# Optimization experiments

Hardware: AMD Instinct MI355X
Metric: run time of the kernel (lower is better)

## Reference

```python
import jax, jax.numpy as jnp
import numpy as np

LRELU = 0.01  # torch nn.LeakyReLU default slope

def _lrelu(x):
    return jnp.where(x >= 0, x, LRELU * x)

def setup_inputs() -> dict:
    key = jax.random.key(0)
    ks = jax.random.split(key, 10)
    B, Cin, Cout, H, W, K, FD, LAT = 16, 256, 256, 64, 64, 3, 128, 128
    y = jax.random.normal(ks[0], (B, Cin, H, W), jnp.float32)
    finger = jax.random.randint(ks[1], (B, FD), 0, 2).astype(jnp.float32)
    ori_weight = jax.random.normal(ks[2], (Cout, Cin, K, K), jnp.float32) * 0.05
    w_mask = jax.random.normal(ks[3], (Cout, Cin, 1, 1), jnp.float32)
    f_weight = ori_weight[None]  # param initialized as 1*ori_weight, shape [1,Cout,Cin,K,K]
    style_w1 = jax.random.normal(ks[4], (LAT, FD), jnp.float32) / np.sqrt(FD)
    style_w2 = jax.random.normal(ks[5], (2 * Cin * K * K, LAT), jnp.float32) / np.sqrt(LAT)
    ori_bias = jax.random.normal(ks[6], (Cout,), jnp.float32) * 0.05
    b_mask = jax.random.normal(ks[7], (Cout,), jnp.float32)
    f_bias = ori_bias[None]  # [1,Cout]
    bias_w1 = jax.random.normal(ks[8], (Cout, FD), jnp.float32) / np.sqrt(FD)
    bias_w2 = jax.random.normal(ks[9], (Cout, Cout), jnp.float32) / np.sqrt(Cout)
    return dict(y=y, finger=finger, ori_weight=ori_weight, w_mask=w_mask,
                f_weight=f_weight, style_w1=style_w1, style_w2=style_w2,
                ori_bias=ori_bias, b_mask=b_mask, f_bias=f_bias,
                bias_w1=bias_w1, bias_w2=bias_w2)

def reference(y, finger, ori_weight, w_mask, f_weight, style_w1, style_w2,
              ori_bias, b_mask, f_bias, bias_w1, bias_w2):
    B = y.shape[0]
    Cout, Cin, K, _ = ori_weight.shape
    relu6 = lambda v: jnp.clip(v, 0.0, 6.0)
    # mask blending coefficients (w_mask broadcasts over the KxK taps, as in .repeat)
    f_w_weight = (6.0 - relu6(w_mask)) / 6.0          # [Cout,Cin,1,1]
    f_w_bias = (6.0 - relu6(b_mask)) / 6.0            # [Cout]
    mean_ori = ori_weight.mean()
    std_ori = jnp.std(ori_weight, ddof=1)             # torch .std() is unbiased
    # ApplyStyle: finger -> LAT -> 2*Cin*K*K scale/shift applied to f_weight
    h = _lrelu(finger @ style_w1.T)                   # [B,LAT]
    style = (h @ style_w2.T).reshape(B, 2, 1, Cin, K, K)
    s_weight = f_weight * (style[:, 0] + 1.0) + style[:, 1]  # [B,Cout,Cin,K,K]
    fw = f_w_weight[None]
    w1 = (1.0 - fw) * ori_weight[None] + fw * s_weight
    # per-sample whole-tensor re-standardization to ori stats
    mean = w1.mean(axis=(1, 2, 3, 4), keepdims=True)
    std = jnp.std(w1, axis=(1, 2, 3, 4), keepdims=True, ddof=1)
    w2 = (w1 - mean) / std * std_ori + mean_ori
    new_weight = (1.0 - fw) * ori_weight[None] + fw * w2      # [B,Cout,Cin,K,K]
    # per-sample bias
    s_bias = f_bias * _lrelu(_lrelu(finger @ bias_w1.T) @ bias_w2.T)  # [B,Cout]
    new_bias = (1.0 - f_w_bias) * ori_bias + f_w_bias * s_bias        # [B,Cout]
    pad = K // 2
    def conv_one(xi, wi, bi):
        o = jax.lax.conv_general_dilated(xi[None], wi, (1, 1),
                                         [(pad, pad), (pad, pad)],
                                         dimension_numbers=('NCHW', 'OIHW', 'NCHW'))
        return o[0] + bi[:, None, None]
    return jax.vmap(conv_one)(y, new_weight, new_bias)   # [B,Cout,H,W]
```

## Files before the change

kernel.cpp:

```cpp
#include <hip/hip_runtime.h>
#include <math.h>

#define LSLOPE 0.01f

__device__ __forceinline__ float lrelu(float x){ return x >= 0.f ? x : LSLOPE * x; }

typedef __attribute__((ext_vector_type(8))) short short8;
typedef __attribute__((ext_vector_type(4))) float f32x4;

__device__ __forceinline__ unsigned short f2bf(float f){
  union { float f; unsigned u; } v; v.f = f;
  unsigned r = v.u + 0x7FFFu + ((v.u >> 16) & 1u);
  return (unsigned short)(r >> 16);
}

__device__ __forceinline__ void gload_lds16(const unsigned short* g, unsigned short* l){
  __builtin_amdgcn_global_load_lds((const __attribute__((address_space(1))) unsigned int*)(g),
                                   (__attribute__((address_space(3))) unsigned int*)(l), 16, 0, 0);
}

constexpr int B    = 16;
constexpr int CIN  = 256;
constexpr int COUT = 256;
constexpr int HH   = 64;
constexpr int WW   = 64;
constexpr int FD   = 128;
constexpr int LAT  = 128;
constexpr int WPS  = CIN * 9;
constexpr int WTOT = COUT * WPS;
constexpr int HP   = 66;

constexpr int OFF_STAT  = 0;
constexpr int OFF_BMEAN = 16;
constexpr int OFF_BSTD  = 32;
constexpr int OFF_P     = 64;
constexpr int OFF_C     = OFF_P + 11 * 8 * WPS;
constexpr int OFF_STYLE = OFF_C + 11 * WPS;
constexpr int OFF_NBIAS = OFF_STYLE + B * 2 * WPS;
constexpr int OFF_NW    = OFF_NBIAS + B * COUT;
constexpr int OFF_YTR   = OFF_NW + (B * 9 * COUT * CIN) / 2;

__global__ __launch_bounds__(256) void k_coeff(const float* __restrict__ ow, const float* __restrict__ fwgt,
                                               const float* __restrict__ wmask, float* __restrict__ P){
  const int rb = blockIdx.x, ob = blockIdx.y;
  const int tid = threadIdx.x;
  const int rem = rb * 256 + tid;
  const int ic = rem / 9;
  float a_ow = 0.f, q_ow = 0.f, ab = 0.f, qb = 0.f;
  float a1 = 0.f, a2 = 0.f, d1 = 0.f, d2 = 0.f, d3 = 0.f, d4 = 0.f, d5 = 0.f;
  for (int oc = ob * 32; oc < ob * 32 + 32; ++oc){
    float w = ow[(size_t)oc * WPS + rem];
    float f = fwgt[(size_t)oc * WPS + rem];
    float m = wmask[oc * CIN + ic];
    float fw = (6.f - fminf(fmaxf(m, 0.f), 6.f)) * (1.f / 6.f);
    float base = w + fw * (f - w);
    float c1 = fw * f, c2 = fw;
    a_ow += w; q_ow += w * w;
    ab += base; qb += base * base;
    a1 += c1; a2 += c2;
    d1 += c1 * c1; d2 += c2 * c2; d3 += base * c1; d4 += base * c2; d5 += c1 * c2;
  }
  float* p = P + (size_t)ob * WPS + rem;
  p[(size_t)0  * 8 * WPS] = a_ow; p[(size_t)1  * 8 * WPS] = q_ow;
  p[(size_t)2  * 8 * WPS] = ab;   p[(size_t)3  * 8 * WPS] = qb;
  p[(size_t)4  * 8 * WPS] = a1;   p[(size_t)5  * 8 * WPS] = a2;
  p[(size_t)6  * 8 * WPS] = d1;   p[(size_t)7  * 8 * WPS] = d2;
  p[(size_t)8  * 8 * WPS] = d3;   p[(size_t)9  * 8 * WPS] = d4;
  p[(size_t)10 * 8 * WPS] = d5;
}

__global__ void k_coeff_r(const float* __restrict__ P, float* __restrict__ C){
  const int rem = blockIdx.x * 256 + threadIdx.x;
  #pragma unroll
  for (int a = 0; a < 11; ++a){
    float v = 0.f;
    for (int ob = 0; ob < 8; ++ob) v += P[((size_t)a * 8 + ob) * WPS + rem];
    C[(size_t)a * WPS + rem] = v;
  }
}

__global__ __launch_bounds__(256) void k_wstats(const float* __restrict__ C, const float* __restrict__ style,
                                                float* stat, float* bmean, float* bstd){
  __shared__ float rs[4][4];
  const int b = blockIdx.x, tid = threadIdx.x;
  const int lane = tid & 63, wid = tid >> 6;
  const float* st = style + (size_t)b * 2 * WPS;
  float s = 0.f, q = 0.f, so = 0.f, qo = 0.f;
  for (int k = 0; k < 9; ++k){
    int rem = k * 256 + tid;
    float aow = C[0 * WPS + rem], qow = C[1 * WPS + rem];
    float ab  = C[2 * WPS + rem], qb  = C[3 * WPS + rem];
    float a1  = C[4 * WPS + rem], a2  = C[5 * WPS + rem];
    float d1  = C[6 * WPS + rem], d2  = C[7 * WPS + rem];
    float d3  = C[8 * WPS + rem], d4  = C[9 * WPS + rem], d5 = C[10 * WPS + rem];
    float s0 = st[rem], s1 = st[WPS + rem];
    so += aow; qo += qow;
    s += ab + s0 * a1 + s1 * a2;
    q += qb + s0 * s0 * d1 + s1 * s1 * d2 + 2.f * (s0 * d3 + s1 * d4 + s0 * s1 * d5);
  }
  for (int o = 32; o > 0; o >>= 1){
    s += __shfl_down(s, o); q += __shfl_down(q, o);
    so += __shfl_down(so, o); qo += __shfl_down(qo, o);
  }
  if (lane == 0){ rs[0][wid] = s; rs[1][wid] = q; rs[2][wid] = so; rs[3][wid] = qo; }
  __syncthreads();
  if (tid == 0){
    const float N = (float)WTOT;
    float S = rs[0][0] + rs[0][1] + rs[0][2] + rs[0][3];
    float Q = rs[1][0] + rs[1][1] + rs[1][2] + rs[1][3];
    bmean[b] = S / N;
    bstd[b]  = sqrtf((Q - S * S / N) / (N - 1.f));
    if (b == 0){
      float SO = rs[2][0] + rs[2][1] + rs[2][2] + rs[2][3];
      float QO = rs[3][0] + rs[3][1] + rs[3][2] + rs[3][3];
      stat[0] = SO / N;
      stat[1] = sqrtf((QO - SO * SO / N) / (N - 1.f));
    }
  }
}

__global__ __launch_bounds__(256) void k_style_bias(const float* __restrict__ finger, const float* __restrict__ sw1,
                                                    const float* __restrict__ sw2, float* __restrict__ style,
                                                    const float* __restrict__ bw1, const float* __restrict__ bw2,
                                                    const float* __restrict__ fbias, const float* __restrict__ bmask,
                                                    const float* __restrict__ obias, float* __restrict__ nbias){
  __shared__ float sh[COUT];
  const int blk = blockIdx.x;
  const int tid = threadIdx.x;
  if (blk < B * 18){
    const int b = blk / 18, j0 = (blk - b * 18) * 256;
    if (tid < LAT){
      float a = 0.f;
      const float* fg = finger + b * FD;
      const float* w = sw1 + (size_t)tid * FD;
      for (int f = 0; f < FD; ++f) a += fg[f] * w[f];
      sh[tid] = lrelu(a);
    }
    __syncthreads();
    const int j = j0 + tid;
    float a = 0.f;
    const float* w2 = sw2 + (size_t)j * LAT;
    for (int l = 0; l < LAT; ++l) a += sh[l] * w2[l];
    style[(size_t)b * 2 * WPS + j] = a;
  } else {
    const int b = blk - B * 18, o = tid;
    float acc = 0.f;
    for (int f = 0; f < FD; ++f) acc += finger[b * FD + f] * bw1[o * FD + f];
    sh[o] = lrelu(acc);
    __syncthreads();
    float t = 0.f;
    for (int c = 0; c < COUT; ++c) t += sh[c] * bw2[o * COUT + c];
    t = lrelu(t);
    float sb = fbias[o] * t;
    float fwb = (6.f - fminf(fmaxf(bmask[o], 0.f), 6.f)) * (1.f / 6.f);
    nbias[b * COUT + o] = (1.f - fwb) * obias[o] + fwb * sb;
  }
}

__global__ __launch_bounds__(256) void k_new_weight4(const float* __restrict__ ow, const float* __restrict__ fwgt,
                                                     const float* __restrict__ wmask, const float* __restrict__ style,
                                                     const float* __restrict__ stat, const float* __restrict__ bmean,
                                                     const float* __restrict__ bstd, unsigned short* __restrict__ nw){
  __shared__ float ows[WPS];
  __shared__ float fws[WPS];
  __shared__ float sts[2 * WPS];
  const int bi = blockIdx.x, oc = blockIdx.y;
  const int tid = threadIdx.x;
  const float mean_ori = stat[0], std_ori = stat[1];
  const float* owr = ow + (size_t)oc * WPS;
  const float* fwr = fwgt + (size_t)oc * WPS;
  for (int i = tid; i < WPS; i += 256){ ows[i] = owr[i]; fws[i] = fwr[i]; }
  const float fw = (6.f - fminf(fmaxf(wmask[oc * CIN + tid], 0.f), 6.f)) * (1.f / 6.f);
  #pragma unroll
  for (int bb = 0; bb < 2; ++bb){
    const int b = bi * 2 + bb;
    __syncthreads();
    const float* st = style + (size_t)b * 2 * WPS;
    for (int i = tid; i < 2 * WPS; i += 256) sts[i] = st[i];
    __syncthreads();
    const float bm = bmean[b], bs = bstd[b];
    #pragma unroll
    for (int t = 0; t < 9; ++t){
      int rem = tid * 9 + t;
      float owv = ows[rem];
      float sw = fws[rem] * (sts[rem] + 1.f) + sts[WPS + rem];
      float w1 = owv + fw * (sw - owv);
      float w2 = (w1 - bm) / bs * std_ori + mean_ori;
      nw[((size_t)(b * 9 + t) * COUT + oc) * CIN + tid] = f2bf(owv + fw * (w2 - owv));
    }
  }
}

constexpr int PADT = 264;
__global__ __launch_bounds__(256) void k_ytrp(const float* __restrict__ y, unsigned short* __restrict__ ytrp){
  __shared__ unsigned short t[64 * PADT];
  const int ghp = blockIdx.x;
  const int b = blockIdx.y;
  const int tid = threadIdx.x;
  unsigned short* dst = ytrp + ((size_t)b * HP + ghp) * HP * CIN;
  if (ghp == 0 || ghp == HP - 1){
    for (int c = tid; c < HP * CIN / 8; c += 256) ((uint4*)dst)[c] = (uint4){0, 0, 0, 0};
    return;
  }
  const int h = ghp - 1;
  const float* src = y + (size_t)b * CIN * HH * WW + h * WW;
  #pragma unroll
  for (int k = 0; k < 16; ++k){
    int idx = tid + k * 256;
    int ic = idx >> 4, w4 = (idx & 15) * 4;
    float4 v = *(const float4*)(src + (size_t)ic * HH * WW + w4);
    t[(w4 + 0) * PADT + ic] = f2bf(v.x);
    t[(w4 + 1) * PADT + ic] = f2bf(v.y);
    t[(w4 + 2) * PADT + ic] = f2bf(v.z);
    t[(w4 + 3) * PADT + ic] = f2bf(v.w);
  }
  __syncthreads();
  for (int c = tid; c < HP * CIN / 8; c += 256){
    int gwp = c >> 5, icg = (c & 31) * 8;
    uint4 v = (uint4){0, 0, 0, 0};
    if (gwp >= 1 && gwp <= 64) v = *(const uint4*)(&t[(gwp - 1) * PADT + icg]);
    ((uint4*)dst)[c] = v;
  }
}

__global__ __launch_bounds__(256, 2) void k_conv_mfma11(const unsigned short* __restrict__ ytrp,
                                                        const unsigned short* __restrict__ nw,
                                                        const float* __restrict__ nbias,
                                                        float* __restrict__ out){
  __shared__ __align__(16) unsigned short Wa[3 * 128 * 32];
  __shared__ __align__(16) unsigned short Yt[288 * 32];
  __shared__ float bsh[128];

  const int bid = blockIdx.x;
  const int xcd = bid & 7;
  const int b   = ((bid >> 8) << 3) | xcd;
  const int oc0 = ((bid >> 3) & 1) * 128;
  const int hwt = (bid >> 4) & 15;
  const int tid = threadIdx.x;
  const int lane = tid & 63, wid = tid >> 6;
  const int wr = wid >> 1, wc = wid & 1;
  const int hw0 = hwt * 256;
  const int h0  = hwt * 4;

  if (tid < 128) bsh[tid] = nbias[b * COUT + oc0 + tid];

  f32x4 acc[4][8];
  #pragma unroll
  for (int i = 0; i < 4; ++i)
    #pragma unroll
    for (int j = 0; j < 8; ++j) acc[i][j] = (f32x4){0.f, 0.f, 0.f, 0.f};

  const unsigned short* nwb = nw + ((size_t)(b * 9) * COUT + oc0) * CIN;
  const unsigned short* ytb = ytrp + (size_t)b * HP * HP * CIN;

  int a_tap[6], a_go[6], a_lo[6];
  #pragma unroll
  for (int s = 0; s < 6; ++s){
    int I = wid + 4 * s;
    int tap = I >> 3, rowbase = (I & 7) * 16;
    int row = rowbase + (lane >> 2), p = lane & 3;
    int g = p ^ ((row >> 1) & 3);
    a_tap[s] = tap;
    a_go[s]  = row * CIN + g * 8;
    a_lo[s]  = (tap * 128 + rowbase) * 32;
  }
  int y_go[5], y_lo[5]; bool y_has[5];
  #pragma unroll
  for (int s = 0; s < 5; ++s){
    int I = wid + 4 * s;
    y_has[s] = (I < 18);
    int Ic = y_has[s] ? I : 0;
    int site = Ic * 16 + (lane >> 2);
    int srow = site / 72;
    int scol = site - srow * 72;
    int gwp  = scol > 65 ? 65 : scol;
    int p = lane & 3, g = p ^ ((site >> 1) & 3);
    y_go[s] = ((h0 + srow + 1) * HP + gwp) * CIN + g * 8;
    y_lo[s] = Ic * 16 * 32;
  }

  const int gq = lane >> 4;
  int a_rb[4];
  #pragma unroll
  for (int mi = 0; mi < 4; ++mi){
    int r = wr * 64 + mi * 16 + (lane & 15);
    a_rb[mi] = r * 64 + ((gq ^ ((r >> 1) & 3)) << 4);
  }
  int b_site[8];
  #pragma unroll
  for (int ni = 0; ni < 8; ++ni)
    b_site[ni] = (wc * 2 + (ni >> 2)) * 72 + (ni & 3) * 16 + (lane & 15);

  #define STAGE(IT)                                                                 \
    {                                                                               \
      const int dhb = (IT) >> 3;                                                    \
      const int ic0s = ((IT) & 7) * 32;                                             \
      const unsigned short* ybase = ytb + (ptrdiff_t)(dhb - 1) * HP * CIN + ic0s;   \
      _Pragma("unroll")                                                             \
      for (int s = 0; s < 5; ++s)                                                   \
        if (y_has[s]) gload_lds16(ybase + y_go[s], &Yt[0] + y_lo[s]);               \
      const unsigned short* atap = nwb + (size_t)(dhb * 3) * COUT * CIN + ic0s;     \
      _Pragma("unroll")                                                             \
      for (int s = 0; s < 6; ++s)                                                   \
        gload_lds16(atap + (size_t)a_tap[s] * COUT * CIN + a_go[s], &Wa[0] + a_lo[s]); \
    }

  #define COMPUTE()                                                                 \
    {                                                                               \
      const char* wap = (const char*)&Wa[0];                                        \
      const char* ytp = (const char*)&Yt[0];                                        \
      _Pragma("unroll")                                                             \
      for (int tap = 0; tap < 3; ++tap){                                            \
        short8 af[4];                                                               \
        _Pragma("unroll")                                                           \
        for (int mi = 0; mi < 4; ++mi)                                              \
          af[mi] = *(const short8*)(wap + tap * 8192 + a_rb[mi]);                   \
        _Pragma("unroll")                                                           \
        for (int ni = 0; ni < 8; ++ni){                                             \
          const int site = b_site[ni] + tap;                                        \
          const int boff = (site << 6) + ((gq ^ ((site >> 1) & 3)) << 4);           \
          const short8 bf = *(const short8*)(ytp + boff);                           \
          _Pragma("unroll")                                                         \
          for (int mi = 0; mi < 4; ++mi)                                            \
            acc[mi][ni] = __builtin_amdgcn_mfma_f32_16x16x32_bf16(af[mi], bf, acc[mi][ni], 0, 0, 0); \
        }                                                                           \
      }                                                                             \
    }

  #pragma unroll 1
  for (int it = 0; it < 24; ++it){
    __syncthreads();
    STAGE(it);
    __syncthreads();
    COMPUTE();
  }
  #undef STAGE
  #undef COMPUTE

  const int col_l = lane & 15, row_l = (lane >> 4) * 4;
  #pragma unroll
  for (int mi = 0; mi < 4; ++mi){
    #pragma unroll
    for (int r = 0; r < 4; ++r){
      const int ocl = wr * 64 + mi * 16 + row_l + r;
      const float bb = bsh[ocl];
      float* op = out + ((size_t)(b * COUT + oc0 + ocl)) * (HH * WW) + hw0 + wc * 128;
      #pragma unroll
      for (int ni = 0; ni < 8; ++ni)
        op[(ni >> 2) * 64 + (ni & 3) * 16 + col_l] = acc[mi][ni][r] + bb;
    }
  }
}

extern "C" void kernel_launch(void* const* d_in, const int* in_sizes, int n_in,
                              void* d_out, int out_size, void* d_ws, size_t ws_size,
                              hipStream_t stream){
  const float* y      = (const float*)d_in[0];
  const float* finger = (const float*)d_in[1];
  const float* ow     = (const float*)d_in[2];
  const float* wmask  = (const float*)d_in[3];
  const float* fwgt   = (const float*)d_in[4];
  const float* sw1    = (const float*)d_in[5];
  const float* sw2    = (const float*)d_in[6];
  const float* obias  = (const float*)d_in[7];
  const float* bmask  = (const float*)d_in[8];
  const float* fbias  = (const float*)d_in[9];
  const float* bw1    = (const float*)d_in[10];
  const float* bw2    = (const float*)d_in[11];
  float* out = (float*)d_out;
  float* ws  = (float*)d_ws;

  float* stat  = ws + OFF_STAT;
  float* bmean = ws + OFF_BMEAN;
  float* bstd  = ws + OFF_BSTD;
  float* P     = ws + OFF_P;
  float* C     = ws + OFF_C;
  float* style = ws + OFF_STYLE;
  float* nbias = ws + OFF_NBIAS;
  unsigned short* nw   = (unsigned short*)(ws + OFF_NW);
  unsigned short* ytrp = (unsigned short*)(ws + OFF_YTR);

  k_coeff<<<dim3(9, 8), 256, 0, stream>>>(ow, fwgt, wmask, P);
  k_coeff_r<<<9, 256, 0, stream>>>(P, C);
  k_style_bias<<<B * 18 + B, 256, 0, stream>>>(finger, sw1, sw2, style, bw1, bw2, fbias, bmask, obias, nbias);
  k_wstats<<<B, 256, 0, stream>>>(C, style, stat, bmean, bstd);
  k_new_weight4<<<dim3(B / 2, COUT), 256, 0, stream>>>(ow, fwgt, wmask, style, stat, bmean, bstd, nw);
  k_ytrp<<<dim3(HP, B), 256, 0, stream>>>(y, ytrp);
  k_conv_mfma11<<<512, 256, 0, stream>>>(ytrp, nw, nbias, out);
}
```

Measured before the change: 143.8 us.

## Double-buffer conv LDS tiles with async global-to-LDS prefetch two stages ahead

The conv kernel now keeps two LDS buffers for weight and input tiles and issues global_load_lds for iteration it+2 while computing iteration it. Raw vmcnt waits and s_barrier replace the two __syncthreads per step, so load latency overlaps MFMA work. LDS use roughly doubles and launch bounds drop to one block per CU, which lowers occupancy. The vmcnt(10) count assumes exactly 10 or 11 loads per stage per thread, and y_has makes that count vary, so the waits may be fragile.

```diff
diff --git a/kernel.cpp b/kernel.cpp
--- a/kernel.cpp
+++ b/kernel.cpp
@@ -223,12 +223,14 @@
   }
 }
 
-__global__ __launch_bounds__(256, 2) void k_conv_mfma11(const unsigned short* __restrict__ ytrp,
+__global__ __launch_bounds__(256, 1) void k_conv_mfma12(const unsigned short* __restrict__ ytrp,
                                                         const unsigned short* __restrict__ nw,
                                                         const float* __restrict__ nbias,
                                                         float* __restrict__ out){
-  __shared__ __align__(16) unsigned short Wa[3 * 128 * 32];
-  __shared__ __align__(16) unsigned short Yt[288 * 32];
+  constexpr int WASTRIDE = 3 * 128 * 32;
+  constexpr int YTSTRIDE = 288 * 32;
+  __shared__ __align__(16) unsigned short Wa[2 * WASTRIDE];
+  __shared__ __align__(16) unsigned short Yt[2 * YTSTRIDE];
   __shared__ float bsh[128];
 
   const int bid = blockIdx.x;
@@ -291,24 +293,26 @@
   for (int ni = 0; ni < 8; ++ni)
     b_site[ni] = (wc * 2 + (ni >> 2)) * 72 + (ni & 3) * 16 + (lane & 15);
 
-  #define STAGE(IT)                                                                 \
+  #define STAGE(BUF, IT)                                                            \
     {                                                                               \
       const int dhb = (IT) >> 3;                                                    \
       const int ic0s = ((IT) & 7) * 32;                                             \
+      unsigned short* wb = &Wa[(BUF) * WASTRIDE];                                   \
+      unsigned short* yb = &Yt[(BUF) * YTSTRIDE];                                   \
       const unsigned short* ybase = ytb + (ptrdiff_t)(dhb - 1) * HP * CIN + ic0s;   \
       _Pragma("unroll")                                                             \
       for (int s = 0; s < 5; ++s)                                                   \
-        if (y_has[s]) gload_lds16(ybase + y_go[s], &Yt[0] + y_lo[s]);               \
+        if (y_has[s]) gload_lds16(ybase + y_go[s], yb + y_lo[s]);                   \
       const unsigned short* atap = nwb + (size_t)(dhb * 3) * COUT * CIN + ic0s;     \
       _Pragma("unroll")                                                             \
       for (int s = 0; s < 6; ++s)                                                   \
-        gload_lds16(atap + (size_t)a_tap[s] * COUT * CIN + a_go[s], &Wa[0] + a_lo[s]); \
-    }
-
-  #define COMPUTE()                                                                 \
+        gload_lds16(atap + (size_t)a_tap[s] * COUT * CIN + a_go[s], wb + a_lo[s]);  \
+    }
+
+  #define COMPUTE(BUF)                                                              \
     {                                                                               \
-      const char* wap = (const char*)&Wa[0];                                        \
-      const char* ytp = (const char*)&Yt[0];                                        \
+      const char* wap = (const char*)&Wa[(BUF) * WASTRIDE];                         \
+      const char* ytp = (const char*)&Yt[(BUF) * YTSTRIDE];                         \
       _Pragma("unroll")                                                             \
       for (int tap = 0; tap < 3; ++tap){                                            \
         short8 af[4];                                                               \
@@ -327,12 +331,16 @@
       }                                                                             \
     }
 
+  STAGE(0, 0);
+  STAGE(1, 1);
   #pragma unroll 1
   for (int it = 0; it < 24; ++it){
-    __syncthreads();
-    STAGE(it);
-    __syncthreads();
-    COMPUTE();
+    if (it < 23) asm volatile("s_waitcnt vmcnt(10)" ::: "memory");
+    else         asm volatile("s_waitcnt vmcnt(0)"  ::: "memory");
+    asm volatile("s_barrier" ::: "memory");
+    COMPUTE(it & 1);
+    asm volatile("s_barrier" ::: "memory");
+    if (it + 2 < 24){ STAGE(it & 1, it + 2); }
   }
   #undef STAGE
   #undef COMPUTE
@@ -386,5 +394,5 @@
   k_wstats<<<B, 256, 0, stream>>>(C, style, stat, bmean, bstd);
   k_new_weight4<<<dim3(B / 2, COUT), 256, 0, stream>>>(ow, fwgt, wmask, style, stat, bmean, bstd, nw);
   k_ytrp<<<dim3(HP, B), 256, 0, stream>>>(y, ytrp);
-  k_conv_mfma11<<<512, 256, 0, stream>>>(ytrp, nw, nbias, out);
-}
+  k_conv_mfma12<<<512, 256, 0, stream>>>(ytrp, nw, nbias, out);
+}
```

After: 166.1 us. 1.16x slower.

## Merge coefficient, style/bias and input-transpose prep into one launch

Applied to the files above, without the earlier changes.

Folds k_coeff, k_coeff_r, k_style_bias and k_ytrp into a single k_prep1 kernel that dispatches on block index. The coefficient sums now loop over all 256 output channels in 9 blocks, so the partial-sum buffer and its separate reduction kernel are gone. The aim is fewer kernel launches and letting the independent prep jobs run concurrently. In exchange, the coefficient work uses only 9 blocks each running a serial 256-iteration loop, which may leave it as a long tail on the critical path.

```diff
diff --git a/kernel.cpp b/kernel.cpp
--- a/kernel.cpp
+++ b/kernel.cpp
@@ -33,49 +33,111 @@
 constexpr int OFF_STAT  = 0;
 constexpr int OFF_BMEAN = 16;
 constexpr int OFF_BSTD  = 32;
-constexpr int OFF_P     = 64;
-constexpr int OFF_C     = OFF_P + 11 * 8 * WPS;
+constexpr int OFF_C     = 64;
 constexpr int OFF_STYLE = OFF_C + 11 * WPS;
 constexpr int OFF_NBIAS = OFF_STYLE + B * 2 * WPS;
 constexpr int OFF_NW    = OFF_NBIAS + B * COUT;
 constexpr int OFF_YTR   = OFF_NW + (B * 9 * COUT * CIN) / 2;
 
-__global__ __launch_bounds__(256) void k_coeff(const float* __restrict__ ow, const float* __restrict__ fwgt,
-                                               const float* __restrict__ wmask, float* __restrict__ P){
-  const int rb = blockIdx.x, ob = blockIdx.y;
+constexpr int PADT = 264;
+constexpr int NB_CF = 9;
+constexpr int NB_SB = B * 18 + B;
+constexpr int NB_YT = HP * B;
+
+__global__ __launch_bounds__(256) void k_prep1(const float* __restrict__ y, unsigned short* __restrict__ ytrp,
+                                               const float* __restrict__ ow, const float* __restrict__ fwgt,
+                                               const float* __restrict__ wmask, float* __restrict__ C,
+                                               const float* __restrict__ finger, const float* __restrict__ sw1,
+                                               const float* __restrict__ sw2, float* __restrict__ style,
+                                               const float* __restrict__ bw1, const float* __restrict__ bw2,
+                                               const float* __restrict__ fbias, const float* __restrict__ bmask,
+                                               const float* __restrict__ obias, float* __restrict__ nbias){
+  __shared__ __align__(16) char shraw[64 * PADT * 2];
+  const int blk = blockIdx.x;
   const int tid = threadIdx.x;
-  const int rem = rb * 256 + tid;
-  const int ic = rem / 9;
-  float a_ow = 0.f, q_ow = 0.f, ab = 0.f, qb = 0.f;
-  float a1 = 0.f, a2 = 0.f, d1 = 0.f, d2 = 0.f, d3 = 0.f, d4 = 0.f, d5 = 0.f;
-  for (int oc = ob * 32; oc < ob * 32 + 32; ++oc){
-    float w = ow[(size_t)oc * WPS + rem];
-    float f = fwgt[(size_t)oc * WPS + rem];
-    float m = wmask[oc * CIN + ic];
-    float fw = (6.f - fminf(fmaxf(m, 0.f), 6.f)) * (1.f / 6.f);
-    float base = w + fw * (f - w);
-    float c1 = fw * f, c2 = fw;
-    a_ow += w; q_ow += w * w;
-    ab += base; qb += base * base;
-    a1 += c1; a2 += c2;
-    d1 += c1 * c1; d2 += c2 * c2; d3 += base * c1; d4 += base * c2; d5 += c1 * c2;
-  }
-  float* p = P + (size_t)ob * WPS + rem;
-  p[(size_t)0  * 8 * WPS] = a_ow; p[(size_t)1  * 8 * WPS] = q_ow;
-  p[(size_t)2  * 8 * WPS] = ab;   p[(size_t)3  * 8 * WPS] = qb;
-  p[(size_t)4  * 8 * WPS] = a1;   p[(size_t)5  * 8 * WPS] = a2;
-  p[(size_t)6  * 8 * WPS] = d1;   p[(size_t)7  * 8 * WPS] = d2;
-  p[(size_t)8  * 8 * WPS] = d3;   p[(size_t)9  * 8 * WPS] = d4;
-  p[(size_t)10 * 8 * WPS] = d5;
-}
-
-__global__ void k_coeff_r(const float* __restrict__ P, float* __restrict__ C){
-  const int rem = blockIdx.x * 256 + threadIdx.x;
-  #pragma unroll
-  for (int a = 0; a < 11; ++a){
-    float v = 0.f;
-    for (int ob = 0; ob < 8; ++ob) v += P[((size_t)a * 8 + ob) * WPS + rem];
-    C[(size_t)a * WPS + rem] = v;
+
+  if (blk < NB_CF){
+    const int rem = blk * 256 + tid;
+    const int ic = rem / 9;
+    float a_ow = 0.f, q_ow = 0.f, ab = 0.f, qb = 0.f;
+    float a1 = 0.f, a2 = 0.f, d1 = 0.f, d2 = 0.f, d3 = 0.f, d4 = 0.f, d5 = 0.f;
+    for (int oc = 0; oc < COUT; ++oc){
+      float w = ow[(size_t)oc * WPS + rem];
+      float f = fwgt[(size_t)oc * WPS + rem];
+      float m = wmask[oc * CIN + ic];
+      float fw = (6.f - fminf(fmaxf(m, 0.f), 6.f)) * (1.f / 6.f);
+      float base = w + fw * (f - w);
+      float c1 = fw * f, c2 = fw;
+      a_ow += w; q_ow += w * w;
+      ab += base; qb += base * base;
+      a1 += c1; a2 += c2;
+      d1 += c1 * c1; d2 += c2 * c2; d3 += base * c1; d4 += base * c2; d5 += c1 * c2;
+    }
+    C[(size_t)0  * WPS + rem] = a_ow; C[(size_t)1  * WPS + rem] = q_ow;
+    C[(size_t)2  * WPS + rem] = ab;   C[(size_t)3  * WPS + rem] = qb;
+    C[(size_t)4  * WPS + rem] = a1;   C[(size_t)5  * WPS + rem] = a2;
+    C[(size_t)6  * WPS + rem] = d1;   C[(size_t)7  * WPS + rem] = d2;
+    C[(size_t)8  * WPS + rem] = d3;   C[(size_t)9  * WPS + rem] = d4;
+    C[(size_t)10 * WPS + rem] = d5;
+  } else if (blk < NB_CF + NB_SB){
+    float* sh = (float*)shraw;
+    const int blk2 = blk - NB_CF;
+    if (blk2 < B * 18){
+      const int b = blk2 / 18, j0 = (blk2 - b * 18) * 256;
+      if (tid < LAT){
+        float a = 0.f;
+        const float* fg = finger + b * FD;
+        const float* w = sw1 + (size_t)tid * FD;
+        for (int f = 0; f < FD; ++f) a += fg[f] * w[f];
+        sh[tid] = lrelu(a);
+      }
+      __syncthreads();
+      const int j = j0 + tid;
+      float a = 0.f;
+      const float* w2 = sw2 + (size_t)j * LAT;
+      for (int l = 0; l < LAT; ++l) a += sh[l] * w2[l];
+      style[(size_t)b * 2 * WPS + j] = a;
+    } else {
+      const int b = blk2 - B * 18, o = tid;
+      float acc = 0.f;
+      for (int f = 0; f < FD; ++f) acc += finger[b * FD + f] * bw1[o * FD + f];
+      sh[o] = lrelu(acc);
+      __syncthreads();
+      float t = 0.f;
+      for (int c = 0; c < COUT; ++c) t += sh[c] * bw2[o * COUT + c];
+      t = lrelu(t);
+      float sb = fbias[o] * t;
+      float fwb = (6.f - fminf(fmaxf(bmask[o], 0.f), 6.f)) * (1.f / 6.f);
+      nbias[b * COUT + o] = (1.f - fwb) * obias[o] + fwb * sb;
+    }
+  } else {
+    unsigned short* t = (unsigned short*)shraw;
+    const int blk3 = blk - NB_CF - NB_SB;
+    const int ghp = blk3 % HP, b = blk3 / HP;
+    unsigned short* dst = ytrp + ((size_t)b * HP + ghp) * HP * CIN;
+    if (ghp == 0 || ghp == HP - 1){
+      for (int c = tid; c < HP * CIN / 8; c += 256) ((uint4*)dst)[c] = (uint4){0, 0, 0, 0};
+      return;
+    }
+    const int h = ghp - 1;
+    const float* src = y + (size_t)b * CIN * HH * WW + h * WW;
+    #pragma unroll
+    for (int k = 0; k < 16; ++k){
+      int idx = tid + k * 256;
+      int ic = idx >> 4, w4 = (idx & 15) * 4;
+      float4 v = *(const float4*)(src + (size_t)ic * HH * WW + w4);
+      t[(w4 + 0) * PADT + ic] = f2bf(v.x);
+      t[(w4 + 1) * PADT + ic] = f2bf(v.y);
+      t[(w4 + 2) * PADT + ic] = f2bf(v.z);
+      t[(w4 + 3) * PADT + ic] = f2bf(v.w);
+    }
+    __syncthreads();
+    for (int c = tid; c < HP * CIN / 8; c += 256){
+      int gwp = c >> 5, icg = (c & 31) * 8;
+      uint4 v = (uint4){0, 0, 0, 0};
+      if (gwp >= 1 && gwp <= 64) v = *(const uint4*)(&t[(gwp - 1) * PADT + icg]);
+      ((uint4*)dst)[c] = v;
+    }
   }
 }
 
@@ -119,44 +181,6 @@
   }
 }
 
-__global__ __launch_bounds__(256) void k_style_bias(const float* __restrict__ finger, const float* __restrict__ sw1,
-                                                    const float* __restrict__ sw2, float* __restrict__ style,
-                                                    const float* __restrict__ bw1, const float* __restrict__ bw2,
-                                                    const float* __restrict__ fbias, const float* __restrict__ bmask,
-                                                    const float* __restrict__ obias, float* __restrict__ nbias){
-  __shared__ float sh[COUT];
-  const int blk = blockIdx.x;
-  const int tid = threadIdx.x;
-  if (blk < B * 18){
-    const int b = blk / 18, j0 = (blk - b * 18) * 256;
-    if (tid < LAT){
-      float a = 0.f;
-      const float* fg = finger + b * FD;
-      const float* w = sw1 + (size_t)tid * FD;
-      for (int f = 0; f < FD; ++f) a += fg[f] * w[f];
-      sh[tid] = lrelu(a);
-    }
-    __syncthreads();
-    const int j = j0 + tid;
-    float a = 0.f;
-    const float* w2 = sw2 + (size_t)j * LAT;
-    for (int l = 0; l < LAT; ++l) a += sh[l] * w2[l];
-    style[(size_t)b * 2 * WPS + j] = a;
-  } else {
-    const int b = blk - B * 18, o = tid;
-    float acc = 0.f;
-    for (int f = 0; f < FD; ++f) acc += finger[b * FD + f] * bw1[o * FD + f];
-    sh[o] = lrelu(acc);
-    __syncthreads();
-    float t = 0.f;
-    for (int c = 0; c < COUT; ++c) t += sh[c] * bw2[o * COUT + c];
-    t = lrelu(t);
-    float sb = fbias[o] * t;
-    float fwb = (6.f - fminf(fmaxf(bmask[o], 0.f), 6.f)) * (1.f / 6.f);
-    nbias[b * COUT + o] = (1.f - fwb) * obias[o] + fwb * sb;
-  }
-}
-
 __global__ __launch_bounds__(256) void k_new_weight4(const float* __restrict__ ow, const float* __restrict__ fwgt,
                                                      const float* __restrict__ wmask, const float* __restrict__ style,
                                                      const float* __restrict__ stat, const float* __restrict__ bmean,
@@ -188,38 +212,6 @@
       float w2 = (w1 - bm) / bs * std_ori + mean_ori;
       nw[((size_t)(b * 9 + t) * COUT + oc) * CIN + tid] = f2bf(owv + fw * (w2 - owv));
     }
-  }
-}
-
-constexpr int PADT = 264;
-__global__ __launch_bounds__(256) void k_ytrp(const float* __restrict__ y, unsigned short* __restrict__ ytrp){
-  __shared__ unsigned short t[64 * PADT];
-  const int ghp = blockIdx.x;
-  const int b = blockIdx.y;
-  const int tid = threadIdx.x;
-  unsigned short* dst = ytrp + ((size_t)b * HP + ghp) * HP * CIN;
-  if (ghp == 0 || ghp == HP - 1){
-    for (int c = tid; c < HP * CIN / 8; c += 256) ((uint4*)dst)[c] = (uint4){0, 0, 0, 0};
-    return;
-  }
-  const int h = ghp - 1;
-  const float* src = y + (size_t)b * CIN * HH * WW + h * WW;
-  #pragma unroll
-  for (int k = 0; k < 16; ++k){
-    int idx = tid + k * 256;
-    int ic = idx >> 4, w4 = (idx & 15) * 4;
-    float4 v = *(const float4*)(src + (size_t)ic * HH * WW + w4);
-    t[(w4 + 0) * PADT + ic] = f2bf(v.x);
-    t[(w4 + 1) * PADT + ic] = f2bf(v.y);
-    t[(w4 + 2) * PADT + ic] = f2bf(v.z);
-    t[(w4 + 3) * PADT + ic] = f2bf(v.w);
-  }
-  __syncthreads();
-  for (int c = tid; c < HP * CIN / 8; c += 256){
-    int gwp = c >> 5, icg = (c & 31) * 8;
-    uint4 v = (uint4){0, 0, 0, 0};
-    if (gwp >= 1 && gwp <= 64) v = *(const uint4*)(&t[(gwp - 1) * PADT + icg]);
-    ((uint4*)dst)[c] = v;
   }
 }
 
@@ -373,18 +365,16 @@
   float* stat  = ws + OFF_STAT;
   float* bmean = ws + OFF_BMEAN;
   float* bstd  = ws + OFF_BSTD;
-  float* P     = ws + OFF_P;
   float* C     = ws + OFF_C;
   float* style = ws + OFF_STYLE;
   float* nbias = ws + OFF_NBIAS;
   unsigned short* nw   = (unsigned short*)(ws + OFF_NW);
   unsigned short* ytrp = (unsigned short*)(ws + OFF_YTR);
 
-  k_coeff<<<dim3(9, 8), 256, 0, stream>>>(ow, fwgt, wmask, P);
-  k_coeff_r<<<9, 256, 0, stream>>>(P, C);
-  k_style_bias<<<B * 18 + B, 256, 0, stream>>>(finger, sw1, sw2, style, bw1, bw2, fbias, bmask, obias, nbias);
+  k_prep1<<<NB_CF + NB_SB + NB_YT, 256, 0, stream>>>(y, ytrp, ow, fwgt, wmask, C,
+                                                     finger, sw1, sw2, style,
+                                                     bw1, bw2, fbias, bmask, obias, nbias);
   k_wstats<<<B, 256, 0, stream>>>(C, style, stat, bmean, bstd);
   k_new_weight4<<<dim3(B / 2, COUT), 256, 0, stream>>>(ow, fwgt, wmask, style, stat, bmean, bstd, nw);
-  k_ytrp<<<dim3(HP, B), 256, 0, stream>>>(y, ytrp);
   k_conv_mfma11<<<512, 256, 0, stream>>>(ytrp, nw, nbias, out);
 }
```

New measurement: 139.9 us. 1.03x faster.
